# Kernel tuning notes

Hardware: AMD Instinct MI355X
Metric: run time of the kernel (lower is better)

## Reference

```python
import jax, jax.numpy as jnp
import numpy as np

NUM_HEADS = 16
NEG = -1e9


def setup_inputs() -> dict:
    key = jax.random.key(0)
    k_x, k_w1, k_w2, k_b, k_p = jax.random.split(key, 5)
    B, T, C = 4, 2048, 1024
    x = jax.random.normal(k_x, (B, T, C), dtype=jnp.float32)
    # nn.Linear default init ~ U(-1/sqrt(fan_in), 1/sqrt(fan_in)); stored as (in, out) for x @ W
    s = 1.0 / np.sqrt(C)
    Wqkv = jax.random.uniform(k_w1, (C, 3 * C), minval=-s, maxval=s, dtype=jnp.float32)
    Wout = jax.random.uniform(k_w2, (C, C), minval=-s, maxval=s, dtype=jnp.float32)
    bout = jax.random.uniform(k_b, (C,), minval=-s, maxval=s, dtype=jnp.float32)
    perm = jax.random.permutation(k_p, T).astype(jnp.int32)
    return {"x": x, "Wqkv": Wqkv, "Wout": Wout, "bout": bout, "perm": perm}


def reference(x, Wqkv, Wout, bout, perm):
    B, T, C = x.shape
    H = NUM_HEADS
    D = C // H
    qkv = x @ Wqkv                                   # [B,T,3C]
    q, k, v = jnp.split(qkv, 3, axis=-1)
    q = q.reshape(B, T, H, D)
    k = k.reshape(B, T, H, D)
    v = v.reshape(B, T, H, D)
    scale = 1.0 / jnp.sqrt(jnp.asarray(D, dtype=x.dtype))
    scores = jnp.einsum('bqhd,bkhd->bhqk', q, k) * scale   # [B,H,T,T]
    # permuted causal mask: allowed[i, j] = tril[i, perm[j]] = (perm[j] <= i)
    i = jnp.arange(T)[:, None]
    bias = jnp.where(perm[None, :] <= i, 0.0, NEG).astype(x.dtype)  # [T,T]
    attn = jax.nn.softmax(scores + bias[None, None, :, :], axis=-1)
    out = jnp.einsum('bhqk,bkhd->bqhd', attn, v).reshape(B, T, C)
    return out @ Wout + bout
```

## Files before the change

### kernel.cpp

```cpp
#include <hip/hip_runtime.h>
#include <stdint.h>
#include <stddef.h>

#define BSZ   4
#define TSEQ  2048
#define CDIM  1024
#define HEADS 16
#define DHEAD 64

typedef __attribute__((ext_vector_type(8))) short v8s;
typedef __attribute__((ext_vector_type(4))) float v4f;

__device__ __forceinline__ v4f mfma16(v8s a, v8s b, v4f c) {
  return __builtin_amdgcn_mfma_f32_16x16x32_bf16(a, b, c, 0, 0, 0);
}

__device__ __forceinline__ short f2bf(float f) {
  union { float f; uint32_t u; } v; v.f = f;
  uint32_t r = (v.u + 0x7FFFu + ((v.u >> 16) & 1u)) >> 16;
  return (short)(uint16_t)r;
}

__device__ __forceinline__ uint32_t cvt_pk_bf16(float lo, float hi) {
  uint32_t r;
  asm("v_cvt_pk_bf16_f32 %0, %1, %2" : "=v"(r) : "v"(lo), "v"(hi));
  return r;
}

__device__ __forceinline__ void gl_lds16(const void* g, void* l) {
  __builtin_amdgcn_global_load_lds((const __attribute__((address_space(1))) void*)g,
                                   (__attribute__((address_space(3))) void*)l, 16, 0, 0);
}

#define BARw __builtin_amdgcn_s_barrier()
#define LGKM0 do { asm volatile("s_waitcnt lgkmcnt(0)" ::: "memory"); \
                   __builtin_amdgcn_sched_barrier(0); } while (0)

__global__ __launch_bounds__(256) void k_convert(const float* __restrict__ in,
                                                 short* __restrict__ out, int n) {
  int i = (blockIdx.x * 256 + threadIdx.x) * 4;
  if (i >= n) return;
  float4 v = *(const float4*)(in + i);
  short4 o;
  o.x = f2bf(v.x); o.y = f2bf(v.y); o.z = f2bf(v.z); o.w = f2bf(v.w);
  *(short4*)(out + i) = o;
}

__global__ __launch_bounds__(256) void k_transpose_conv(const float* __restrict__ in,
                                                        short* __restrict__ out,
                                                        int R, int C) {
  __shared__ float tile[32][33];
  int c0 = blockIdx.x * 32, r0 = blockIdx.y * 32;
  int tx = threadIdx.x, ty = threadIdx.y;
  #pragma unroll
  for (int i = ty; i < 32; i += 8)
    tile[i][tx] = in[(size_t)(r0 + i) * C + c0 + tx];
  __syncthreads();
  #pragma unroll
  for (int i = ty; i < 32; i += 8)
    out[(size_t)(c0 + i) * R + r0 + tx] = f2bf(tile[tx][i]);
}

__global__ __launch_bounds__(256) void k_vt(const short* __restrict__ Vs,
                                            short* __restrict__ Vt) {
  __shared__ short tl[64][72];
  const int t0 = blockIdx.x * 64, h = blockIdx.y, b = blockIdx.z;
  const int row = threadIdx.x >> 2, c4 = threadIdx.x & 3;
  const short* src = Vs + (size_t)(b * TSEQ + t0 + row) * CDIM + h * DHEAD;
  #pragma unroll
  for (int it = 0; it < 2; ++it) {
    int ch = c4 + it * 4;
    *(v8s*)&tl[row][ch * 8] = *(const v8s*)(src + ch * 8);
  }
  __syncthreads();
  short* dst = Vt + ((size_t)(b * HEADS + h) * DHEAD + row) * TSEQ + t0;
  #pragma unroll
  for (int it = 0; it < 2; ++it) {
    int ch = c4 + it * 4;
    v8s o;
    #pragma unroll
    for (int j = 0; j < 8; ++j) o[j] = tl[ch * 8 + j][row];
    *(v8s*)(dst + ch * 8) = o;
  }
}

__global__ __launch_bounds__(512, 2) void k_gemm_qkv(const short* __restrict__ A,
                                                     const short* __restrict__ Wt,
                                                     const int* __restrict__ perm,
                                                     short* __restrict__ QK,
                                                     short* __restrict__ Vs) {
  __shared__ __align__(16) short Alds[2][256 * 64];
  __shared__ __align__(16) short Blds[2][256 * 64];
  const int l = threadIdx.x & 63, w = threadIdx.x >> 6;
  const int lr = l & 15, lg = l >> 4;
  const int wm = w >> 2, wn = w & 3;
  const int bid = blockIdx.x;
  const int swz = (bid & 7) * 48 + (bid >> 3);
  const int by = swz / 12, bx = swz - by * 12;
  const int row0 = by * 256, col0 = bx * 256;

  v4f acc[8][4];
  #pragma unroll
  for (int i = 0; i < 8; ++i)
    #pragma unroll
    for (int j = 0; j < 4; ++j) acc[i][j] = (v4f){0.f, 0.f, 0.f, 0.f};

  const int rowoff = w * 8 + (l >> 3);
  const int gch = ((l & 7) ^ (l >> 3)) * 16;
  const char* Asrc = (const char*)A  + (size_t)(row0 + rowoff) * 2048 + gch;
  const char* Bsrc = (const char*)Wt + (size_t)(col0 + rowoff) * 2048 + gch;
  char* AL = (char*)&Alds[0][0];
  char* BL = (char*)&Blds[0][0];
  const int sdst = w * 1024;

  auto SA = [&](int kt, int h, int d) {
    char* dst = AL + d * 32768 + h * 16384 + sdst;
    const char* s = Asrc + (size_t)(h * 128) * 2048 + kt * 128;
    gl_lds16(s, dst);
    gl_lds16(s + (size_t)64 * 2048, dst + 8192);
  };
  auto SB = [&](int kt, int h, int d) {
    char* dst = BL + d * 32768 + h * 16384 + sdst;
    const char* s = Bsrc + (size_t)(h * 128) * 2048 + kt * 128;
    gl_lds16(s, dst);
    gl_lds16(s + (size_t)64 * 2048, dst + 8192);
  };

  const int rsw = (lr & 7) * 16;
  const int koff0 = (lg * 16) ^ rsw;
  const int koff1 = ((4 + lg) * 16) ^ rsw;
  const int abase = (wm * 128 + lr) * 128;
  const int bbase = (wn * 64 + lr) * 128;

  v8s af[4][2], bf[4][2];
  auto RDA = [&](int d, int ih) {
    const char* base = AL + d * 32768 + abase + ih * 8192;
    #pragma unroll
    for (int ii = 0; ii < 4; ++ii) {
      af[ii][0] = *(const v8s*)(base + ii * 2048 + koff0);
      af[ii][1] = *(const v8s*)(base + ii * 2048 + koff1);
    }
  };
  auto RDB = [&](int d) {
    const char* base = BL + d * 32768 + bbase;
    #pragma unroll
    for (int j = 0; j < 4; ++j) {
      bf[j][0] = *(const v8s*)(base + j * 2048 + koff0);
      bf[j][1] = *(const v8s*)(base + j * 2048 + koff1);
    }
  };

#define MMC(IH, JH)                                                            \
  do {                                                                         \
    __builtin_amdgcn_s_setprio(1);                                             \
    _Pragma("unroll")                                                          \
    for (int kk = 0; kk < 2; ++kk)                                             \
      _Pragma("unroll")                                                        \
      for (int ii = 0; ii < 4; ++ii)                                           \
        _Pragma("unroll")                                                      \
        for (int jj = 0; jj < 2; ++jj)                                         \
          acc[(IH) * 4 + ii][(JH) * 2 + jj] =                                  \
              mfma16(af[ii][kk], bf[(JH) * 2 + jj][kk],                        \
                     acc[(IH) * 4 + ii][(JH) * 2 + jj]);                       \
    __builtin_amdgcn_s_setprio(0);                                             \
  } while (0)

  SB(0, 0, 0); SB(0, 1, 0); SA(0, 0, 0); SA(0, 1, 0);
  SB(1, 0, 1); SB(1, 1, 1); SA(1, 0, 1); SA(1, 1, 1);
  asm volatile("s_waitcnt vmcnt(8)" ::: "memory");
  BARw;

  for (int i = 0; i < 8; ++i) {
    const int kt2 = 2 * i + 2, kt3 = 2 * i + 3;
    const bool st = (i < 7);
    RDA(0, 0); RDB(0);
    BARw; LGKM0; MMC(0, 0); BARw;
    if (st) SB(kt2, 0, 0);
    BARw; MMC(0, 1); BARw;
    RDA(0, 1); if (st) SB(kt2, 1, 0);
    BARw; LGKM0; MMC(1, 0); BARw;
    if (st) { SA(kt2, 0, 0); asm volatile("s_waitcnt vmcnt(6)" ::: "memory"); }
    else    { asm volatile("s_waitcnt vmcnt(0)" ::: "memory"); }
    BARw; MMC(1, 1); BARw;
    RDA(1, 0); RDB(1); if (st) SA(kt2, 1, 0);
    BARw; LGKM0; MMC(0, 0); BARw;
    if (st) SB(kt3, 0, 1);
    BARw; MMC(0, 1); BARw;
    RDA(1, 1); if (st) SB(kt3, 1, 1);
    BARw; LGKM0; MMC(1, 0); BARw;
    if (st) {
      SA(kt3, 0, 1); SA(kt3, 1, 1);
      asm volatile("s_waitcnt vmcnt(8)" ::: "memory");
    }
    BARw; MMC(1, 1); BARw;
  }
#undef MMC

  const int region = (col0 + wn * 64) >> 10;
  if (region == 0) {
    #pragma unroll
    for (int i = 0; i < 8; ++i) {
      int rowb = row0 + wm * 128 + i * 16 + lg * 4;
      #pragma unroll
      for (int j = 0; j < 4; ++j) {
        int col = col0 + wn * 64 + j * 16 + lr;
        #pragma unroll
        for (int r = 0; r < 4; ++r)
          QK[(size_t)(rowb + r) * 2048 + col] = f2bf(acc[i][j][r]);
      }
    }
  } else if (region == 1) {
    #pragma unroll
    for (int i = 0; i < 8; ++i) {
      int rowb = row0 + wm * 128 + i * 16 + lg * 4;
      int prow[4];
      #pragma unroll
      for (int r = 0; r < 4; ++r) {
        int t = (rowb + r) & 2047;
        prow[r] = ((rowb + r) - t) + perm[t];
      }
      #pragma unroll
      for (int j = 0; j < 4; ++j) {
        int col = col0 + wn * 64 + j * 16 + lr;
        #pragma unroll
        for (int r = 0; r < 4; ++r)
          QK[(size_t)prow[r] * 2048 + col] = f2bf(acc[i][j][r]);
      }
    }
  } else {
    #pragma unroll
    for (int i = 0; i < 8; ++i) {
      int rowb = row0 + wm * 128 + i * 16 + lg * 4;
      int prow[4];
      #pragma unroll
      for (int r = 0; r < 4; ++r) {
        int t = (rowb + r) & 2047;
        prow[r] = ((rowb + r) - t) + perm[t];
      }
      #pragma unroll
      for (int j = 0; j < 4; ++j) {
        int vc = col0 + wn * 64 + j * 16 + lr - 2048;
        #pragma unroll
        for (int r = 0; r < 4; ++r)
          Vs[(size_t)prow[r] * CDIM + vc] = f2bf(acc[i][j][r]);
      }
    }
  }
}

__global__ __launch_bounds__(256) void k_gemm_out(const short* __restrict__ A,
                                                  const short* __restrict__ Wt,
                                                  const float* __restrict__ bias,
                                                  float* __restrict__ out) {
  __shared__ __align__(16) short As[3][128 * 32];
  __shared__ __align__(16) short Bs[3][128 * 32];
  int l = threadIdx.x & 63, w = threadIdx.x >> 6;
  int lr = l & 15, lg = l >> 4;
  int row0 = blockIdx.y * 128, col0 = blockIdx.x * 128;
  int wr = (w >> 1) * 64, wc = (w & 1) * 64;
  v4f acc[4][4];
  #pragma unroll
  for (int i = 0; i < 4; ++i)
    #pragma unroll
    for (int j = 0; j < 4; ++j) acc[i][j] = (v4f){0.f, 0.f, 0.f, 0.f};

  const short* Ag = A  + (size_t)(row0 + w * 32 + (l >> 2)) * CDIM + (l & 3) * 8;
  const short* Bg = Wt + (size_t)(col0 + w * 32 + (l >> 2)) * CDIM + (l & 3) * 8;
  const int so = (w * 32) * 32;

  auto STAGE = [&](int it, int bf) {
    int k0 = it * 32;
    gl_lds16(Ag + k0, &As[bf][so]);
    gl_lds16(Ag + k0 + 16 * CDIM, &As[bf][so + 16 * 32]);
    gl_lds16(Bg + k0, &Bs[bf][so]);
    gl_lds16(Bg + k0 + 16 * CDIM, &Bs[bf][so + 16 * 32]);
  };

  auto BODY = [&](int it, int cur) {
    if (it < 31) asm volatile("s_waitcnt vmcnt(4)" ::: "memory");
    else         asm volatile("s_waitcnt vmcnt(0)" ::: "memory");
    __builtin_amdgcn_s_barrier();
    if (it < 30) STAGE(it + 2, (cur + 2) % 3);
    v8s af[4], bfr[4];
    #pragma unroll
    for (int i = 0; i < 4; ++i) af[i] = *(const v8s*)&As[cur][(wr + i * 16 + lr) * 32 + lg * 8];
    #pragma unroll
    for (int j = 0; j < 4; ++j) bfr[j] = *(const v8s*)&Bs[cur][(wc + j * 16 + lr) * 32 + lg * 8];
    __builtin_amdgcn_s_setprio(1);
    #pragma unroll
    for (int i = 0; i < 4; ++i)
      #pragma unroll
      for (int j = 0; j < 4; ++j) acc[i][j] = mfma16(af[i], bfr[j], acc[i][j]);
    __builtin_amdgcn_s_setprio(0);
  };

  STAGE(0, 0);
  STAGE(1, 1);
  for (int it = 0; it < 30; it += 3) {
    BODY(it, 0); BODY(it + 1, 1); BODY(it + 2, 2);
  }
  BODY(30, 0);
  BODY(31, 1);

  #pragma unroll
  for (int i = 0; i < 4; ++i) {
    int rowb = row0 + wr + i * 16 + lg * 4;
    #pragma unroll
    for (int j = 0; j < 4; ++j) {
      int col = col0 + wc + j * 16 + lr;
      float bv = bias[col];
      #pragma unroll
      for (int r = 0; r < 4; ++r)
        out[(size_t)(rowb + r) * CDIM + col] = acc[i][j][r] + bv;
    }
  }
}

__global__ __launch_bounds__(512) void k_flash(const short* __restrict__ QK,
                                               const short* __restrict__ Vt,
                                               short* __restrict__ O) {
  __shared__ __align__(16) short Kbuf[3][64 * 64];
  __shared__ __align__(16) short Vbuf[3][64 * 64];
  __shared__ __align__(16) short plds[8][32 * 64];
  const int l = threadIdx.x & 63, w = threadIdx.x >> 6;
  const int lr = l & 15, lg = l >> 4;
  const int n = blockIdx.x;
  const int u = n & 255;
  const int h = u & 15;
  const int b = (u >> 4) & 3;
  const int qi = u >> 6;
  const int qb = (n < 256) ? (7 - qi) : qi;
  const int q0 = qb * 256 + w * 32;
  const int nt = 4 * qb + 4;
  const float C1 = 0.18033688011112042f;

  const short* Qb = QK + (size_t)(b * TSEQ + q0) * 2048 + h * DHEAD;
  v8s aq[2][2];
  #pragma unroll
  for (int hh = 0; hh < 2; ++hh) {
    aq[hh][0] = *(const v8s*)(Qb + (size_t)(hh * 16 + lr) * 2048 + lg * 8);
    aq[hh][1] = *(const v8s*)(Qb + (size_t)(hh * 16 + lr) * 2048 + 32 + lg * 8);
  }

  v8s ones;
  #pragma unroll
  for (int i = 0; i < 8; ++i) ones[i] = (short)0x3F80;

  v4f Oacc[2][4], sacc[2];
  #pragma unroll
  for (int hh = 0; hh < 2; ++hh) {
    sacc[hh] = (v4f){0.f, 0.f, 0.f, 0.f};
    #pragma unroll
    for (int d = 0; d < 4; ++d) Oacc[hh][d] = (v4f){0.f, 0.f, 0.f, 0.f};
  }

  const char* Ksrc = (const char*)QK + (size_t)(b * TSEQ) * 4096 + 2048 + (size_t)h * 128;
  const char* Vsrc = (const char*)Vt + (size_t)((b * HEADS + h) * DHEAD) * 4096;
  const int srow = w * 8 + (l >> 3);
  const int csw  = ((l & 7) ^ (l >> 3)) * 16;

  auto STAGE = [&](int kt, int bf) {
    char* kd = (char*)&Kbuf[bf][0] + w * 1024;
    char* vd = (char*)&Vbuf[bf][0] + w * 1024;
    gl_lds16(Ksrc + ((size_t)kt * 64 + srow) * 4096 + csw, kd);
    gl_lds16(Vsrc + (size_t)srow * 4096 + (size_t)kt * 128 + csw, vd);
  };

  STAGE(0, 0);
  if (nt > 1) STAGE(1, 1);
  const int x16 = (lr & 7) * 16;
  char* pb = (char*)&plds[w][0];
  const int e7 = lr & 7;

  for (int kt = 0; kt < nt; ++kt) {
    const int cur = kt % 3;
    if (kt + 1 < nt) asm volatile("s_waitcnt vmcnt(2)" ::: "memory");
    else             asm volatile("s_waitcnt vmcnt(0)" ::: "memory");
    __builtin_amdgcn_s_barrier();
    if (kt + 2 < nt) STAGE(kt + 2, (kt + 2) % 3);

    if (kt * 64 <= q0 + 31) {
      const char* Kc = (const char*)&Kbuf[cur][0];
      const char* Vc = (const char*)&Vbuf[cur][0];

      v4f S[2][4];
      __builtin_amdgcn_s_setprio(1);
      #pragma unroll
      for (int g = 0; g < 4; ++g) {
        const char* rp = Kc + (g * 16 + lr) * 128;
        v8s k0 = *(const v8s*)(rp + ((lg * 16) ^ x16));
        v8s k1 = *(const v8s*)(rp + ((64 + lg * 16) ^ x16));
        #pragma unroll
        for (int hh = 0; hh < 2; ++hh) {
          v4f z = (v4f){0.f, 0.f, 0.f, 0.f};
          z = mfma16(k0, aq[hh][0], z);
          S[hh][g] = mfma16(k1, aq[hh][1], z);
        }
      }
      __builtin_amdgcn_s_setprio(0);

      if (kt * 64 + 63 <= q0) {
        #pragma unroll
        for (int hh = 0; hh < 2; ++hh) {
          char* rowp = pb + (hh * 16 + lr) * 128 + 8 * (lg & 1);
          #pragma unroll
          for (int g = 0; g < 4; ++g) {
            float p0 = __builtin_exp2f(fmaf(S[hh][g][0], C1, -8.0f));
            float p1 = __builtin_exp2f(fmaf(S[hh][g][1], C1, -8.0f));
            float p2 = __builtin_exp2f(fmaf(S[hh][g][2], C1, -8.0f));
            float p3 = __builtin_exp2f(fmaf(S[hh][g][3], C1, -8.0f));
            uint2 wv;
            wv.x = cvt_pk_bf16(p0, p1);
            wv.y = cvt_pk_bf16(p2, p3);
            *(uint2*)(rowp + (((2 * g + (lg >> 1)) ^ e7) << 4)) = wv;
          }
        }
      } else {
        const int kg0 = kt * 64 + lg * 4;
        #pragma unroll
        for (int hh = 0; hh < 2; ++hh) {
          const int irow = q0 + hh * 16 + lr;
          char* rowp = pb + (hh * 16 + lr) * 128 + 8 * (lg & 1);
          #pragma unroll
          for (int g = 0; g < 4; ++g) {
            float p[4];
            #pragma unroll
            for (int r = 0; r < 4; ++r) {
              float e = __builtin_exp2f(fmaf(S[hh][g][r], C1, -8.0f));
              p[r] = (kg0 + g * 16 + r <= irow) ? e : 0.0f;
            }
            uint2 wv;
            wv.x = cvt_pk_bf16(p[0], p[1]);
            wv.y = cvt_pk_bf16(p[2], p[3]);
            *(uint2*)(rowp + (((2 * g + (lg >> 1)) ^ e7) << 4)) = wv;
          }
        }
      }
      asm volatile("s_waitcnt lgkmcnt(0)" ::: "memory");
      __builtin_amdgcn_sched_barrier(0);

      v8s ap[2][2];
      #pragma unroll
      for (int hh = 0; hh < 2; ++hh) {
        const char* rowp = pb + (hh * 16 + lr) * 128;
        ap[hh][0] = *(const v8s*)(rowp + ((lg ^ e7) << 4));
        ap[hh][1] = *(const v8s*)(rowp + (((4 + lg) ^ e7) << 4));
      }
      __builtin_amdgcn_s_setprio(1);
      #pragma unroll
      for (int hh = 0; hh < 2; ++hh) {
        sacc[hh] = mfma16(ap[hh][0], ones, sacc[hh]);
        sacc[hh] = mfma16(ap[hh][1], ones, sacc[hh]);
      }
      #pragma unroll
      for (int dk = 0; dk < 4; ++dk) {
        const char* vp = Vc + (dk * 16 + lr) * 128;
        v8s bv0 = *(const v8s*)(vp + ((lg * 16) ^ x16));
        v8s bv1 = *(const v8s*)(vp + ((64 + lg * 16) ^ x16));
        #pragma unroll
        for (int hh = 0; hh < 2; ++hh) {
          Oacc[hh][dk] = mfma16(ap[hh][0], bv0, Oacc[hh][dk]);
          Oacc[hh][dk] = mfma16(ap[hh][1], bv1, Oacc[hh][dk]);
        }
      }
      __builtin_amdgcn_s_setprio(0);
    }
  }

  #pragma unroll
  for (int hh = 0; hh < 2; ++hh) {
    float inv[4];
    #pragma unroll
    for (int r = 0; r < 4; ++r) inv[r] = 1.0f / sacc[hh][r];
    #pragma unroll
    for (int dk = 0; dk < 4; ++dk)
      #pragma unroll
      for (int r = 0; r < 4; ++r) {
        int row = q0 + hh * 16 + lg * 4 + r;
        int col = h * DHEAD + dk * 16 + lr;
        O[(size_t)(b * TSEQ + row) * CDIM + col] = f2bf(Oacc[hh][dk][r] * inv[r]);
      }
  }
}

extern "C" void kernel_launch(void* const* d_in, const int* in_sizes, int n_in,
                              void* d_out, int out_size, void* d_ws, size_t ws_size,
                              hipStream_t stream) {
  const float* x    = (const float*)d_in[0];
  const float* Wqkv = (const float*)d_in[1];
  const float* Wout = (const float*)d_in[2];
  const float* bout = (const float*)d_in[3];
  const int*   perm = (const int*)d_in[4];
  float* out = (float*)d_out;

  uint8_t* ws = (uint8_t*)d_ws;
  const size_t NTOK = (size_t)BSZ * TSEQ;
  size_t off = 0;
  short* Xb    = (short*)(ws + off); off += NTOK * CDIM * 2;
  short* Wqkvt = (short*)(ws + off); off += (size_t)3 * CDIM * CDIM * 2;
  short* Woutt = (short*)(ws + off); off += (size_t)CDIM * CDIM * 2;
  short* QKb   = (short*)(ws + off); off += NTOK * 2048 * 2;
  short* Vtb   = (short*)(ws + off); off += NTOK * CDIM * 2;
  short* Obuf  = (short*)(ws + off); off += NTOK * CDIM * 2;
  short* Vsb   = Obuf;

  {
    int n = (int)(NTOK * CDIM);
    k_convert<<<n / (256 * 4), 256, 0, stream>>>(x, Xb, n);
  }
  k_transpose_conv<<<dim3(3 * CDIM / 32, CDIM / 32), dim3(32, 8), 0, stream>>>(Wqkv, Wqkvt, CDIM, 3 * CDIM);
  k_transpose_conv<<<dim3(CDIM / 32, CDIM / 32), dim3(32, 8), 0, stream>>>(Wout, Woutt, CDIM, CDIM);
  k_gemm_qkv<<<dim3((NTOK / 256) * (3 * CDIM / 256)), 512, 0, stream>>>(Xb, Wqkvt, perm, QKb, Vsb);
  k_vt<<<dim3(TSEQ / 64, HEADS, BSZ), 256, 0, stream>>>(Vsb, Vtb);
  k_flash<<<dim3(512), 512, 0, stream>>>(QKb, Vtb, Obuf);
  k_gemm_out<<<dim3(CDIM / 128, NTOK / 128), 256, 0, stream>>>(Obuf, Woutt, bout, out);
}
```

Baseline: 201.4 us.

## Load K/V fragments directly from global memory in flash kernel, smaller blocks

The flash attention kernel stops staging K and V tiles through a triple-buffered shared-memory pipeline with barriers. Each wave now reads its MFMA K and V fragments straight from global memory (relying on L2/cache reuse) and loops only over its own causal extent. Blocks shrink to 256 threads covering 128 query rows, launched as 1024 blocks with a new load-balancing order. This removes barriers and shared-memory traffic but exposes global-load latency in the MFMA loop, and K/V data is no longer shared across the waves of a block.

New measurement: 244.6 us. +21.4%, slower.

```diff
diff --git a/kernel.cpp b/kernel.cpp
--- a/kernel.cpp
+++ b/kernel.cpp
@@ -316,22 +316,21 @@
   }
 }
 
-__global__ __launch_bounds__(512) void k_flash(const short* __restrict__ QK,
+__global__ __launch_bounds__(256) void k_flash(const short* __restrict__ QK,
                                                const short* __restrict__ Vt,
                                                short* __restrict__ O) {
-  __shared__ __align__(16) short Kbuf[3][64 * 64];
-  __shared__ __align__(16) short Vbuf[3][64 * 64];
-  __shared__ __align__(16) short plds[8][32 * 64];
+  __shared__ __align__(16) short plds[4][32 * 64];
   const int l = threadIdx.x & 63, w = threadIdx.x >> 6;
   const int lr = l & 15, lg = l >> 4;
   const int n = blockIdx.x;
+  const int g = n >> 8;
   const int u = n & 255;
   const int h = u & 15;
   const int b = (u >> 4) & 3;
-  const int qi = u >> 6;
-  const int qb = (n < 256) ? (7 - qi) : qi;
-  const int q0 = qb * 256 + w * 32;
-  const int nt = 4 * qb + 4;
+  const int s = u >> 6;
+  const int qb = (g == 0) ? (15 - s) : (g == 1) ? s : (g == 2) ? (11 - s) : (4 + s);
+  const int q0 = qb * 128 + w * 32;
+  const int nt_w = ((q0 + 31) >> 6) + 1;
   const float C1 = 0.18033688011112042f;
 
   const short* Qb = QK + (size_t)(b * TSEQ + q0) * 2048 + h * DHEAD;
@@ -354,116 +353,92 @@
     for (int d = 0; d < 4; ++d) Oacc[hh][d] = (v4f){0.f, 0.f, 0.f, 0.f};
   }
 
-  const char* Ksrc = (const char*)QK + (size_t)(b * TSEQ) * 4096 + 2048 + (size_t)h * 128;
-  const char* Vsrc = (const char*)Vt + (size_t)((b * HEADS + h) * DHEAD) * 4096;
-  const int srow = w * 8 + (l >> 3);
-  const int csw  = ((l & 7) ^ (l >> 3)) * 16;
-
-  auto STAGE = [&](int kt, int bf) {
-    char* kd = (char*)&Kbuf[bf][0] + w * 1024;
-    char* vd = (char*)&Vbuf[bf][0] + w * 1024;
-    gl_lds16(Ksrc + ((size_t)kt * 64 + srow) * 4096 + csw, kd);
-    gl_lds16(Vsrc + (size_t)srow * 4096 + (size_t)kt * 128 + csw, vd);
-  };
-
-  STAGE(0, 0);
-  if (nt > 1) STAGE(1, 1);
-  const int x16 = (lr & 7) * 16;
+  const short* Klane = QK + (size_t)(b * TSEQ) * 2048 + 1024 + h * DHEAD
+                          + (size_t)lr * 2048 + lg * 8;
+  const short* Vlane = Vt + (size_t)((b * HEADS + h) * DHEAD) * TSEQ
+                          + (size_t)lr * TSEQ + lg * 8;
+
   char* pb = (char*)&plds[w][0];
   const int e7 = lr & 7;
 
-  for (int kt = 0; kt < nt; ++kt) {
-    const int cur = kt % 3;
-    if (kt + 1 < nt) asm volatile("s_waitcnt vmcnt(2)" ::: "memory");
-    else             asm volatile("s_waitcnt vmcnt(0)" ::: "memory");
-    __builtin_amdgcn_s_barrier();
-    if (kt + 2 < nt) STAGE(kt + 2, (kt + 2) % 3);
-
-    if (kt * 64 <= q0 + 31) {
-      const char* Kc = (const char*)&Kbuf[cur][0];
-      const char* Vc = (const char*)&Vbuf[cur][0];
-
-      v4f S[2][4];
-      __builtin_amdgcn_s_setprio(1);
-      #pragma unroll
-      for (int g = 0; g < 4; ++g) {
-        const char* rp = Kc + (g * 16 + lr) * 128;
-        v8s k0 = *(const v8s*)(rp + ((lg * 16) ^ x16));
-        v8s k1 = *(const v8s*)(rp + ((64 + lg * 16) ^ x16));
+  for (int kt = 0; kt < nt_w; ++kt) {
+    const short* Kt = Klane + (size_t)kt * 64 * 2048;
+    const short* Vtp = Vlane + kt * 64;
+
+    v4f S[2][4];
+    #pragma unroll
+    for (int g4 = 0; g4 < 4; ++g4) {
+      v8s k0 = *(const v8s*)(Kt + (size_t)g4 * 16 * 2048);
+      v8s k1 = *(const v8s*)(Kt + (size_t)g4 * 16 * 2048 + 32);
+      #pragma unroll
+      for (int hh = 0; hh < 2; ++hh) {
+        v4f z = (v4f){0.f, 0.f, 0.f, 0.f};
+        z = mfma16(k0, aq[hh][0], z);
+        S[hh][g4] = mfma16(k1, aq[hh][1], z);
+      }
+    }
+
+    if (kt * 64 + 63 <= q0) {
+      #pragma unroll
+      for (int hh = 0; hh < 2; ++hh) {
+        char* rowp = pb + (hh * 16 + lr) * 128 + 8 * (lg & 1);
         #pragma unroll
-        for (int hh = 0; hh < 2; ++hh) {
-          v4f z = (v4f){0.f, 0.f, 0.f, 0.f};
-          z = mfma16(k0, aq[hh][0], z);
-          S[hh][g] = mfma16(k1, aq[hh][1], z);
+        for (int g4 = 0; g4 < 4; ++g4) {
+          float p0 = __builtin_exp2f(fmaf(S[hh][g4][0], C1, -8.0f));
+          float p1 = __builtin_exp2f(fmaf(S[hh][g4][1], C1, -8.0f));
+          float p2 = __builtin_exp2f(fmaf(S[hh][g4][2], C1, -8.0f));
+          float p3 = __builtin_exp2f(fmaf(S[hh][g4][3], C1, -8.0f));
+          uint2 wv;
+          wv.x = cvt_pk_bf16(p0, p1);
+          wv.y = cvt_pk_bf16(p2, p3);
+          *(uint2*)(rowp + (((2 * g4 + (lg >> 1)) ^ e7) << 4)) = wv;
         }
       }
-      __builtin_amdgcn_s_setprio(0);
-
-      if (kt * 64 + 63 <= q0) {
+    } else {
+      const int kg0 = kt * 64 + lg * 4;
+      #pragma unroll
+      for (int hh = 0; hh < 2; ++hh) {
+        const int irow = q0 + hh * 16 + lr;
+        char* rowp = pb + (hh * 16 + lr) * 128 + 8 * (lg & 1);
         #pragma unroll
-        for (int hh = 0; hh < 2; ++hh) {
-          char* rowp = pb + (hh * 16 + lr) * 128 + 8 * (lg & 1);
+        for (int g4 = 0; g4 < 4; ++g4) {
+          float p[4];
           #pragma unroll
-          for (int g = 0; g < 4; ++g) {
-            float p0 = __builtin_exp2f(fmaf(S[hh][g][0], C1, -8.0f));
-            float p1 = __builtin_exp2f(fmaf(S[hh][g][1], C1, -8.0f));
-            float p2 = __builtin_exp2f(fmaf(S[hh][g][2], C1, -8.0f));
-            float p3 = __builtin_exp2f(fmaf(S[hh][g][3], C1, -8.0f));
-            uint2 wv;
-            wv.x = cvt_pk_bf16(p0, p1);
-            wv.y = cvt_pk_bf16(p2, p3);
-            *(uint2*)(rowp + (((2 * g + (lg >> 1)) ^ e7) << 4)) = wv;
+          for (int r = 0; r < 4; ++r) {
+            float e = __builtin_exp2f(fmaf(S[hh][g4][r], C1, -8.0f));
+            p[r] = (kg0 + g4 * 16 + r <= irow) ? e : 0.0f;
           }
+          uint2 wv;
+          wv.x = cvt_pk_bf16(p[0], p[1]);
+          wv.y = cvt_pk_bf16(p[2], p[3]);
+          *(uint2*)(rowp + (((2 * g4 + (lg >> 1)) ^ e7) << 4)) = wv;
         }
-      } else {
-        const int kg0 = kt * 64 + lg * 4;
-        #pragma unroll
-        for (int hh = 0; hh < 2; ++hh) {
-          const int irow = q0 + hh * 16 + lr;
-          char* rowp = pb + (hh * 16 + lr) * 128 + 8 * (lg & 1);
-          #pragma unroll
-          for (int g = 0; g < 4; ++g) {
-            float p[4];
-            #pragma unroll
-            for (int r = 0; r < 4; ++r) {
-              float e = __builtin_exp2f(fmaf(S[hh][g][r], C1, -8.0f));
-              p[r] = (kg0 + g * 16 + r <= irow) ? e : 0.0f;
-            }
-            uint2 wv;
-            wv.x = cvt_pk_bf16(p[0], p[1]);
-            wv.y = cvt_pk_bf16(p[2], p[3]);
-            *(uint2*)(rowp + (((2 * g + (lg >> 1)) ^ e7) << 4)) = wv;
-          }
-        }
-      }
-      asm volatile("s_waitcnt lgkmcnt(0)" ::: "memory");
-      __builtin_amdgcn_sched_barrier(0);
-
-      v8s ap[2][2];
+      }
+    }
+    asm volatile("s_waitcnt lgkmcnt(0)" ::: "memory");
+    __builtin_amdgcn_sched_barrier(0);
+
+    v8s ap[2][2];
+    #pragma unroll
+    for (int hh = 0; hh < 2; ++hh) {
+      const char* rowp = pb + (hh * 16 + lr) * 128;
+      ap[hh][0] = *(const v8s*)(rowp + ((lg ^ e7) << 4));
+      ap[hh][1] = *(const v8s*)(rowp + (((4 + lg) ^ e7) << 4));
+    }
+    #pragma unroll
+    for (int hh = 0; hh < 2; ++hh) {
+      sacc[hh] = mfma16(ap[hh][0], ones, sacc[hh]);
+      sacc[hh] = mfma16(ap[hh][1], ones, sacc[hh]);
+    }
+    #pragma unroll
+    for (int dk = 0; dk < 4; ++dk) {
+      v8s bv0 = *(const v8s*)(Vtp + (size_t)dk * 16 * TSEQ);
+      v8s bv1 = *(const v8s*)(Vtp + (size_t)dk * 16 * TSEQ + 32);
       #pragma unroll
       for (int hh = 0; hh < 2; ++hh) {
-        const char* rowp = pb + (hh * 16 + lr) * 128;
-        ap[hh][0] = *(const v8s*)(rowp + ((lg ^ e7) << 4));
-        ap[hh][1] = *(const v8s*)(rowp + (((4 + lg) ^ e7) << 4));
-      }
-      __builtin_amdgcn_s_setprio(1);
-      #pragma unroll
-      for (int hh = 0; hh < 2; ++hh) {
-        sacc[hh] = mfma16(ap[hh][0], ones, sacc[hh]);
-        sacc[hh] = mfma16(ap[hh][1], ones, sacc[hh]);
-      }
-      #pragma unroll
-      for (int dk = 0; dk < 4; ++dk) {
-        const char* vp = Vc + (dk * 16 + lr) * 128;
-        v8s bv0 = *(const v8s*)(vp + ((lg * 16) ^ x16));
-        v8s bv1 = *(const v8s*)(vp + ((64 + lg * 16) ^ x16));
-        #pragma unroll
-        for (int hh = 0; hh < 2; ++hh) {
-          Oacc[hh][dk] = mfma16(ap[hh][0], bv0, Oacc[hh][dk]);
-          Oacc[hh][dk] = mfma16(ap[hh][1], bv1, Oacc[hh][dk]);
-        }
-      }
-      __builtin_amdgcn_s_setprio(0);
+        Oacc[hh][dk] = mfma16(ap[hh][0], bv0, Oacc[hh][dk]);
+        Oacc[hh][dk] = mfma16(ap[hh][1], bv1, Oacc[hh][dk]);
+      }
     }
   }
 
@@ -512,6 +487,6 @@
   k_transpose_conv<<<dim3(CDIM / 32, CDIM / 32), dim3(32, 8), 0, stream>>>(Wout, Woutt, CDIM, CDIM);
   k_gemm_qkv<<<dim3((NTOK / 256) * (3 * CDIM / 256)), 512, 0, stream>>>(Xb, Wqkvt, perm, QKb, Vsb);
   k_vt<<<dim3(TSEQ / 64, HEADS, BSZ), 256, 0, stream>>>(Vsb, Vtb);
-  k_flash<<<dim3(512), 512, 0, stream>>>(QKb, Vtb, Obuf);
+  k_flash<<<dim3(1024), 256, 0, stream>>>(QKb, Vtb, Obuf);
   k_gemm_out<<<dim3(CDIM / 128, NTOK / 128), 256, 0, stream>>>(Obuf, Woutt, bout, out);
 }
```

## Give each flash-attention wave 64 query rows with 4 waves per block

Applied to the files above, without the earlier changes.

The flash kernel now runs 4 waves of 256 threads instead of 8 waves of 512. Each wave owns 64 query rows, handled as two 32-row passes over every K/V tile, and each thread stages two 16-byte chunks per matrix per tile. Each K/V fragment read from LDS now serves more query rows, and fewer waves contend at the per-tile barrier. The cost is more accumulator registers per thread and fewer waves to hide latency, which may reduce occupancy.

After: 247.3 us. +22.8%, slower.

```diff
diff --git a/kernel.cpp b/kernel.cpp
--- a/kernel.cpp
+++ b/kernel.cpp
@@ -316,12 +316,12 @@
   }
 }
 
-__global__ __launch_bounds__(512) void k_flash(const short* __restrict__ QK,
+__global__ __launch_bounds__(256) void k_flash(const short* __restrict__ QK,
                                                const short* __restrict__ Vt,
                                                short* __restrict__ O) {
   __shared__ __align__(16) short Kbuf[3][64 * 64];
   __shared__ __align__(16) short Vbuf[3][64 * 64];
-  __shared__ __align__(16) short plds[8][32 * 64];
+  __shared__ __align__(16) short plds[4][64 * 64];
   const int l = threadIdx.x & 63, w = threadIdx.x >> 6;
   const int lr = l & 15, lg = l >> 4;
   const int n = blockIdx.x;
@@ -330,28 +330,28 @@
   const int b = (u >> 4) & 3;
   const int qi = u >> 6;
   const int qb = (n < 256) ? (7 - qi) : qi;
-  const int q0 = qb * 256 + w * 32;
+  const int q0 = qb * 256 + w * 64;
   const int nt = 4 * qb + 4;
   const float C1 = 0.18033688011112042f;
 
   const short* Qb = QK + (size_t)(b * TSEQ + q0) * 2048 + h * DHEAD;
-  v8s aq[2][2];
-  #pragma unroll
-  for (int hh = 0; hh < 2; ++hh) {
-    aq[hh][0] = *(const v8s*)(Qb + (size_t)(hh * 16 + lr) * 2048 + lg * 8);
-    aq[hh][1] = *(const v8s*)(Qb + (size_t)(hh * 16 + lr) * 2048 + 32 + lg * 8);
+  v8s aq[4][2];
+  #pragma unroll
+  for (int ph = 0; ph < 4; ++ph) {
+    aq[ph][0] = *(const v8s*)(Qb + (size_t)(ph * 16 + lr) * 2048 + lg * 8);
+    aq[ph][1] = *(const v8s*)(Qb + (size_t)(ph * 16 + lr) * 2048 + 32 + lg * 8);
   }
 
   v8s ones;
   #pragma unroll
   for (int i = 0; i < 8; ++i) ones[i] = (short)0x3F80;
 
-  v4f Oacc[2][4], sacc[2];
-  #pragma unroll
-  for (int hh = 0; hh < 2; ++hh) {
-    sacc[hh] = (v4f){0.f, 0.f, 0.f, 0.f};
-    #pragma unroll
-    for (int d = 0; d < 4; ++d) Oacc[hh][d] = (v4f){0.f, 0.f, 0.f, 0.f};
+  v4f Oacc[4][4], sacc[4];
+  #pragma unroll
+  for (int ph = 0; ph < 4; ++ph) {
+    sacc[ph] = (v4f){0.f, 0.f, 0.f, 0.f};
+    #pragma unroll
+    for (int d = 0; d < 4; ++d) Oacc[ph][d] = (v4f){0.f, 0.f, 0.f, 0.f};
   }
 
   const char* Ksrc = (const char*)QK + (size_t)(b * TSEQ) * 4096 + 2048 + (size_t)h * 128;
@@ -362,123 +362,133 @@
   auto STAGE = [&](int kt, int bf) {
     char* kd = (char*)&Kbuf[bf][0] + w * 1024;
     char* vd = (char*)&Vbuf[bf][0] + w * 1024;
-    gl_lds16(Ksrc + ((size_t)kt * 64 + srow) * 4096 + csw, kd);
-    gl_lds16(Vsrc + (size_t)srow * 4096 + (size_t)kt * 128 + csw, vd);
+    const char* ks = Ksrc + ((size_t)kt * 64 + srow) * 4096 + csw;
+    const char* vs = Vsrc + (size_t)srow * 4096 + (size_t)kt * 128 + csw;
+    gl_lds16(ks, kd);
+    gl_lds16(ks + (size_t)32 * 4096, kd + 4096);
+    gl_lds16(vs, vd);
+    gl_lds16(vs + (size_t)32 * 4096, vd + 4096);
   };
 
   STAGE(0, 0);
-  if (nt > 1) STAGE(1, 1);
+  STAGE(1, 1);
   const int x16 = (lr & 7) * 16;
   char* pb = (char*)&plds[w][0];
   const int e7 = lr & 7;
 
   for (int kt = 0; kt < nt; ++kt) {
     const int cur = kt % 3;
-    if (kt + 1 < nt) asm volatile("s_waitcnt vmcnt(2)" ::: "memory");
+    if (kt + 1 < nt) asm volatile("s_waitcnt vmcnt(4)" ::: "memory");
     else             asm volatile("s_waitcnt vmcnt(0)" ::: "memory");
     __builtin_amdgcn_s_barrier();
     if (kt + 2 < nt) STAGE(kt + 2, (kt + 2) % 3);
 
-    if (kt * 64 <= q0 + 31) {
+    if (kt * 64 <= q0 + 63) {
       const char* Kc = (const char*)&Kbuf[cur][0];
       const char* Vc = (const char*)&Vbuf[cur][0];
 
-      v4f S[2][4];
-      __builtin_amdgcn_s_setprio(1);
-      #pragma unroll
-      for (int g = 0; g < 4; ++g) {
-        const char* rp = Kc + (g * 16 + lr) * 128;
-        v8s k0 = *(const v8s*)(rp + ((lg * 16) ^ x16));
-        v8s k1 = *(const v8s*)(rp + ((64 + lg * 16) ^ x16));
-        #pragma unroll
-        for (int hh = 0; hh < 2; ++hh) {
-          v4f z = (v4f){0.f, 0.f, 0.f, 0.f};
-          z = mfma16(k0, aq[hh][0], z);
-          S[hh][g] = mfma16(k1, aq[hh][1], z);
-        }
-      }
-      __builtin_amdgcn_s_setprio(0);
-
-      if (kt * 64 + 63 <= q0) {
-        #pragma unroll
-        for (int hh = 0; hh < 2; ++hh) {
-          char* rowp = pb + (hh * 16 + lr) * 128 + 8 * (lg & 1);
+      #pragma unroll
+      for (int p = 0; p < 2; ++p) {
+        const int q0p = q0 + p * 32;
+        if (kt * 64 > q0p + 31) continue;
+
+        v4f S[2][4];
+        __builtin_amdgcn_s_setprio(1);
+        #pragma unroll
+        for (int g4 = 0; g4 < 4; ++g4) {
+          const char* rp = Kc + (g4 * 16 + lr) * 128;
+          v8s k0 = *(const v8s*)(rp + ((lg * 16) ^ x16));
+          v8s k1 = *(const v8s*)(rp + ((64 + lg * 16) ^ x16));
           #pragma unroll
-          for (int g = 0; g < 4; ++g) {
-            float p0 = __builtin_exp2f(fmaf(S[hh][g][0], C1, -8.0f));
-            float p1 = __builtin_exp2f(fmaf(S[hh][g][1], C1, -8.0f));
-            float p2 = __builtin_exp2f(fmaf(S[hh][g][2], C1, -8.0f));
-            float p3 = __builtin_exp2f(fmaf(S[hh][g][3], C1, -8.0f));
-            uint2 wv;
-            wv.x = cvt_pk_bf16(p0, p1);
-            wv.y = cvt_pk_bf16(p2, p3);
-            *(uint2*)(rowp + (((2 * g + (lg >> 1)) ^ e7) << 4)) = wv;
+          for (int hh = 0; hh < 2; ++hh) {
+            v4f z = (v4f){0.f, 0.f, 0.f, 0.f};
+            z = mfma16(k0, aq[2 * p + hh][0], z);
+            S[hh][g4] = mfma16(k1, aq[2 * p + hh][1], z);
           }
         }
-      } else {
-        const int kg0 = kt * 64 + lg * 4;
-        #pragma unroll
-        for (int hh = 0; hh < 2; ++hh) {
-          const int irow = q0 + hh * 16 + lr;
-          char* rowp = pb + (hh * 16 + lr) * 128 + 8 * (lg & 1);
+        __builtin_amdgcn_s_setprio(0);
+
+        if (kt * 64 + 63 <= q0p) {
           #pragma unroll
-          for (int g = 0; g < 4; ++g) {
-            float p[4];
+          for (int hh = 0; hh < 2; ++hh) {
+            char* rowp = pb + (p * 32 + hh * 16 + lr) * 128 + 8 * (lg & 1);
             #pragma unroll
-            for (int r = 0; r < 4; ++r) {
-              float e = __builtin_exp2f(fmaf(S[hh][g][r], C1, -8.0f));
-              p[r] = (kg0 + g * 16 + r <= irow) ? e : 0.0f;
+            for (int g4 = 0; g4 < 4; ++g4) {
+              float p0 = __builtin_exp2f(fmaf(S[hh][g4][0], C1, -8.0f));
+              float p1 = __builtin_exp2f(fmaf(S[hh][g4][1], C1, -8.0f));
+              float p2 = __builtin_exp2f(fmaf(S[hh][g4][2], C1, -8.0f));
+              float p3 = __builtin_exp2f(fmaf(S[hh][g4][3], C1, -8.0f));
+              uint2 wv;
+              wv.x = cvt_pk_bf16(p0, p1);
+              wv.y = cvt_pk_bf16(p2, p3);
+              *(uint2*)(rowp + (((2 * g4 + (lg >> 1)) ^ e7) << 4)) = wv;
             }
-            uint2 wv;
-            wv.x = cvt_pk_bf16(p[0], p[1]);
-            wv.y = cvt_pk_bf16(p[2], p[3]);
-            *(uint2*)(rowp + (((2 * g + (lg >> 1)) ^ e7) << 4)) = wv;
+          }
+        } else {
+          const int kg0 = kt * 64 + lg * 4;
+          #pragma unroll
+          for (int hh = 0; hh < 2; ++hh) {
+            const int irow = q0p + hh * 16 + lr;
+            char* rowp = pb + (p * 32 + hh * 16 + lr) * 128 + 8 * (lg & 1);
+            #pragma unroll
+            for (int g4 = 0; g4 < 4; ++g4) {
+              float pv[4];
+              #pragma unroll
+              for (int r = 0; r < 4; ++r) {
+                float e = __builtin_exp2f(fmaf(S[hh][g4][r], C1, -8.0f));
+                pv[r] = (kg0 + g4 * 16 + r <= irow) ? e : 0.0f;
+              }
+              uint2 wv;
+              wv.x = cvt_pk_bf16(pv[0], pv[1]);
+              wv.y = cvt_pk_bf16(pv[2], pv[3]);
+              *(uint2*)(rowp + (((2 * g4 + (lg >> 1)) ^ e7) << 4)) = wv;
+            }
           }
         }
-      }
-      asm volatile("s_waitcnt lgkmcnt(0)" ::: "memory");
-      __builtin_amdgcn_sched_barrier(0);
-
-      v8s ap[2][2];
-      #pragma unroll
-      for (int hh = 0; hh < 2; ++hh) {
-        const char* rowp = pb + (hh * 16 + lr) * 128;
-        ap[hh][0] = *(const v8s*)(rowp + ((lg ^ e7) << 4));
-        ap[hh][1] = *(const v8s*)(rowp + (((4 + lg) ^ e7) << 4));
-      }
-      __builtin_amdgcn_s_setprio(1);
-      #pragma unroll
-      for (int hh = 0; hh < 2; ++hh) {
-        sacc[hh] = mfma16(ap[hh][0], ones, sacc[hh]);
-        sacc[hh] = mfma16(ap[hh][1], ones, sacc[hh]);
-      }
-      #pragma unroll
-      for (int dk = 0; dk < 4; ++dk) {
-        const char* vp = Vc + (dk * 16 + lr) * 128;
-        v8s bv0 = *(const v8s*)(vp + ((lg * 16) ^ x16));
-        v8s bv1 = *(const v8s*)(vp + ((64 + lg * 16) ^ x16));
+        asm volatile("s_waitcnt lgkmcnt(0)" ::: "memory");
+        __builtin_amdgcn_sched_barrier(0);
+
+        v8s ap[2][2];
         #pragma unroll
         for (int hh = 0; hh < 2; ++hh) {
-          Oacc[hh][dk] = mfma16(ap[hh][0], bv0, Oacc[hh][dk]);
-          Oacc[hh][dk] = mfma16(ap[hh][1], bv1, Oacc[hh][dk]);
+          const char* rowp = pb + (p * 32 + hh * 16 + lr) * 128;
+          ap[hh][0] = *(const v8s*)(rowp + ((lg ^ e7) << 4));
+          ap[hh][1] = *(const v8s*)(rowp + (((4 + lg) ^ e7) << 4));
         }
-      }
-      __builtin_amdgcn_s_setprio(0);
-    }
-  }
-
-  #pragma unroll
-  for (int hh = 0; hh < 2; ++hh) {
+        __builtin_amdgcn_s_setprio(1);
+        #pragma unroll
+        for (int hh = 0; hh < 2; ++hh) {
+          sacc[2 * p + hh] = mfma16(ap[hh][0], ones, sacc[2 * p + hh]);
+          sacc[2 * p + hh] = mfma16(ap[hh][1], ones, sacc[2 * p + hh]);
+        }
+        #pragma unroll
+        for (int dk = 0; dk < 4; ++dk) {
+          const char* vp = Vc + (dk * 16 + lr) * 128;
+          v8s bv0 = *(const v8s*)(vp + ((lg * 16) ^ x16));
+          v8s bv1 = *(const v8s*)(vp + ((64 + lg * 16) ^ x16));
+          #pragma unroll
+          for (int hh = 0; hh < 2; ++hh) {
+            Oacc[2 * p + hh][dk] = mfma16(ap[hh][0], bv0, Oacc[2 * p + hh][dk]);
+            Oacc[2 * p + hh][dk] = mfma16(ap[hh][1], bv1, Oacc[2 * p + hh][dk]);
+          }
+        }
+        __builtin_amdgcn_s_setprio(0);
+      }
+    }
+  }
+
+  #pragma unroll
+  for (int ph = 0; ph < 4; ++ph) {
     float inv[4];
     #pragma unroll
-    for (int r = 0; r < 4; ++r) inv[r] = 1.0f / sacc[hh][r];
+    for (int r = 0; r < 4; ++r) inv[r] = 1.0f / sacc[ph][r];
     #pragma unroll
     for (int dk = 0; dk < 4; ++dk)
       #pragma unroll
       for (int r = 0; r < 4; ++r) {
-        int row = q0 + hh * 16 + lg * 4 + r;
+        int row = q0 + ph * 16 + lg * 4 + r;
         int col = h * DHEAD + dk * 16 + lr;
-        O[(size_t)(b * TSEQ + row) * CDIM + col] = f2bf(Oacc[hh][dk][r] * inv[r]);
+        O[(size_t)(b * TSEQ + row) * CDIM + col] = f2bf(Oacc[ph][dk][r] * inv[r]);
       }
   }
 }
@@ -512,6 +522,6 @@
   k_transpose_conv<<<dim3(CDIM / 32, CDIM / 32), dim3(32, 8), 0, stream>>>(Wout, Woutt, CDIM, CDIM);
   k_gemm_qkv<<<dim3((NTOK / 256) * (3 * CDIM / 256)), 512, 0, stream>>>(Xb, Wqkvt, perm, QKb, Vsb);
   k_vt<<<dim3(TSEQ / 64, HEADS, BSZ), 256, 0, stream>>>(Vsb, Vtb);
-  k_flash<<<dim3(512), 512, 0, stream>>>(QKb, Vtb, Obuf);
+  k_flash<<<dim3(512), 256, 0, stream>>>(QKb, Vtb, Obuf);
   k_gemm_out<<<dim3(CDIM / 128, NTOK / 128), 256, 0, stream>>>(Obuf, Woutt, bout, out);
 }
```

## Software-pipeline flash loop: overlap next tile's QK^T with current softmax/PV

Applied to the files above, without the earlier changes.

Restructures the attention main loop into a two-stage software pipeline. The QK^T MFMAs for the next K tile now run alongside the softmax and PV of the current tile, using ping-pong score registers. It also adds an occupancy hint to launch_bounds. The intent is to hide exp/LDS latency behind matrix work. The cost is extra registers for a second score tile and vmcnt(0) waits that drain the prefetch, which may reduce memory overlap.

After: 438.3 us. 118% more time.

```diff
diff --git a/kernel.cpp b/kernel.cpp
--- a/kernel.cpp
+++ b/kernel.cpp
@@ -316,9 +316,9 @@
   }
 }
 
-__global__ __launch_bounds__(512) void k_flash(const short* __restrict__ QK,
-                                               const short* __restrict__ Vt,
-                                               short* __restrict__ O) {
+__global__ __launch_bounds__(512, 4) void k_flash(const short* __restrict__ QK,
+                                                  const short* __restrict__ Vt,
+                                                  short* __restrict__ O) {
   __shared__ __align__(16) short Kbuf[3][64 * 64];
   __shared__ __align__(16) short Vbuf[3][64 * 64];
   __shared__ __align__(16) short plds[8][32 * 64];
@@ -366,105 +366,115 @@
     gl_lds16(Vsrc + (size_t)srow * 4096 + (size_t)kt * 128 + csw, vd);
   };
 
-  STAGE(0, 0);
-  if (nt > 1) STAGE(1, 1);
   const int x16 = (lr & 7) * 16;
   char* pb = (char*)&plds[w][0];
   const int e7 = lr & 7;
 
-  for (int kt = 0; kt < nt; ++kt) {
-    const int cur = kt % 3;
-    if (kt + 1 < nt) asm volatile("s_waitcnt vmcnt(2)" ::: "memory");
-    else             asm volatile("s_waitcnt vmcnt(0)" ::: "memory");
-    __builtin_amdgcn_s_barrier();
-    if (kt + 2 < nt) STAGE(kt + 2, (kt + 2) % 3);
-
-    if (kt * 64 <= q0 + 31) {
-      const char* Kc = (const char*)&Kbuf[cur][0];
-      const char* Vc = (const char*)&Vbuf[cur][0];
-
-      v4f S[2][4];
-      __builtin_amdgcn_s_setprio(1);
-      #pragma unroll
-      for (int g = 0; g < 4; ++g) {
-        const char* rp = Kc + (g * 16 + lr) * 128;
-        v8s k0 = *(const v8s*)(rp + ((lg * 16) ^ x16));
-        v8s k1 = *(const v8s*)(rp + ((64 + lg * 16) ^ x16));
+  auto QKT = [&](int t, v4f (&S)[2][4]) {
+    const char* Kc = (const char*)&Kbuf[t % 3][0];
+    __builtin_amdgcn_s_setprio(1);
+    #pragma unroll
+    for (int g = 0; g < 4; ++g) {
+      const char* rp = Kc + (g * 16 + lr) * 128;
+      v8s k0 = *(const v8s*)(rp + ((lg * 16) ^ x16));
+      v8s k1 = *(const v8s*)(rp + ((64 + lg * 16) ^ x16));
+      #pragma unroll
+      for (int hh = 0; hh < 2; ++hh) {
+        v4f z = (v4f){0.f, 0.f, 0.f, 0.f};
+        z = mfma16(k0, aq[hh][0], z);
+        S[hh][g] = mfma16(k1, aq[hh][1], z);
+      }
+    }
+    __builtin_amdgcn_s_setprio(0);
+  };
+
+  auto SMPV = [&](int t, v4f (&S)[2][4]) {
+    if (t * 64 + 63 <= q0) {
+      #pragma unroll
+      for (int hh = 0; hh < 2; ++hh) {
+        char* rowp = pb + (hh * 16 + lr) * 128 + 8 * (lg & 1);
         #pragma unroll
-        for (int hh = 0; hh < 2; ++hh) {
-          v4f z = (v4f){0.f, 0.f, 0.f, 0.f};
-          z = mfma16(k0, aq[hh][0], z);
-          S[hh][g] = mfma16(k1, aq[hh][1], z);
+        for (int g = 0; g < 4; ++g) {
+          float p0 = __builtin_exp2f(fmaf(S[hh][g][0], C1, -8.0f));
+          float p1 = __builtin_exp2f(fmaf(S[hh][g][1], C1, -8.0f));
+          float p2 = __builtin_exp2f(fmaf(S[hh][g][2], C1, -8.0f));
+          float p3 = __builtin_exp2f(fmaf(S[hh][g][3], C1, -8.0f));
+          uint2 wv;
+          wv.x = cvt_pk_bf16(p0, p1);
+          wv.y = cvt_pk_bf16(p2, p3);
+          *(uint2*)(rowp + (((2 * g + (lg >> 1)) ^ e7) << 4)) = wv;
         }
       }
-      __builtin_amdgcn_s_setprio(0);
-
-      if (kt * 64 + 63 <= q0) {
+    } else {
+      const int kg0 = t * 64 + lg * 4;
+      #pragma unroll
+      for (int hh = 0; hh < 2; ++hh) {
+        const int irow = q0 + hh * 16 + lr;
+        char* rowp = pb + (hh * 16 + lr) * 128 + 8 * (lg & 1);
         #pragma unroll
-        for (int hh = 0; hh < 2; ++hh) {
-          char* rowp = pb + (hh * 16 + lr) * 128 + 8 * (lg & 1);
+        for (int g = 0; g < 4; ++g) {
+          float p[4];
           #pragma unroll
-          for (int g = 0; g < 4; ++g) {
-            float p0 = __builtin_exp2f(fmaf(S[hh][g][0], C1, -8.0f));
-            float p1 = __builtin_exp2f(fmaf(S[hh][g][1], C1, -8.0f));
-            float p2 = __builtin_exp2f(fmaf(S[hh][g][2], C1, -8.0f));
-            float p3 = __builtin_exp2f(fmaf(S[hh][g][3], C1, -8.0f));
-            uint2 wv;
-            wv.x = cvt_pk_bf16(p0, p1);
-            wv.y = cvt_pk_bf16(p2, p3);
-            *(uint2*)(rowp + (((2 * g + (lg >> 1)) ^ e7) << 4)) = wv;
+          for (int r = 0; r < 4; ++r) {
+            float e = __builtin_exp2f(fmaf(S[hh][g][r], C1, -8.0f));
+            p[r] = (kg0 + g * 16 + r <= irow) ? e : 0.0f;
           }
+          uint2 wv;
+          wv.x = cvt_pk_bf16(p[0], p[1]);
+          wv.y = cvt_pk_bf16(p[2], p[3]);
+          *(uint2*)(rowp + (((2 * g + (lg >> 1)) ^ e7) << 4)) = wv;
         }
-      } else {
-        const int kg0 = kt * 64 + lg * 4;
-        #pragma unroll
-        for (int hh = 0; hh < 2; ++hh) {
-          const int irow = q0 + hh * 16 + lr;
-          char* rowp = pb + (hh * 16 + lr) * 128 + 8 * (lg & 1);
-          #pragma unroll
-          for (int g = 0; g < 4; ++g) {
-            float p[4];
-            #pragma unroll
-            for (int r = 0; r < 4; ++r) {
-              float e = __builtin_exp2f(fmaf(S[hh][g][r], C1, -8.0f));
-              p[r] = (kg0 + g * 16 + r <= irow) ? e : 0.0f;
-            }
-            uint2 wv;
-            wv.x = cvt_pk_bf16(p[0], p[1]);
-            wv.y = cvt_pk_bf16(p[2], p[3]);
-            *(uint2*)(rowp + (((2 * g + (lg >> 1)) ^ e7) << 4)) = wv;
-          }
-        }
-      }
-      asm volatile("s_waitcnt lgkmcnt(0)" ::: "memory");
-      __builtin_amdgcn_sched_barrier(0);
-
-      v8s ap[2][2];
+      }
+    }
+    asm volatile("s_waitcnt lgkmcnt(0)" ::: "memory");
+    __builtin_amdgcn_sched_barrier(0);
+
+    v8s ap[2][2];
+    #pragma unroll
+    for (int hh = 0; hh < 2; ++hh) {
+      const char* rowp = pb + (hh * 16 + lr) * 128;
+      ap[hh][0] = *(const v8s*)(rowp + ((lg ^ e7) << 4));
+      ap[hh][1] = *(const v8s*)(rowp + (((4 + lg) ^ e7) << 4));
+    }
+    const char* Vc = (const char*)&Vbuf[t % 3][0];
+    __builtin_amdgcn_s_setprio(1);
+    #pragma unroll
+    for (int hh = 0; hh < 2; ++hh) {
+      sacc[hh] = mfma16(ap[hh][0], ones, sacc[hh]);
+      sacc[hh] = mfma16(ap[hh][1], ones, sacc[hh]);
+    }
+    #pragma unroll
+    for (int dk = 0; dk < 4; ++dk) {
+      const char* vp = Vc + (dk * 16 + lr) * 128;
+      v8s bv0 = *(const v8s*)(vp + ((lg * 16) ^ x16));
+      v8s bv1 = *(const v8s*)(vp + ((64 + lg * 16) ^ x16));
       #pragma unroll
       for (int hh = 0; hh < 2; ++hh) {
-        const char* rowp = pb + (hh * 16 + lr) * 128;
-        ap[hh][0] = *(const v8s*)(rowp + ((lg ^ e7) << 4));
-        ap[hh][1] = *(const v8s*)(rowp + (((4 + lg) ^ e7) << 4));
-      }
-      __builtin_amdgcn_s_setprio(1);
-      #pragma unroll
-      for (int hh = 0; hh < 2; ++hh) {
-        sacc[hh] = mfma16(ap[hh][0], ones, sacc[hh]);
-        sacc[hh] = mfma16(ap[hh][1], ones, sacc[hh]);
-      }
-      #pragma unroll
-      for (int dk = 0; dk < 4; ++dk) {
-        const char* vp = Vc + (dk * 16 + lr) * 128;
-        v8s bv0 = *(const v8s*)(vp + ((lg * 16) ^ x16));
-        v8s bv1 = *(const v8s*)(vp + ((64 + lg * 16) ^ x16));
-        #pragma unroll
-        for (int hh = 0; hh < 2; ++hh) {
-          Oacc[hh][dk] = mfma16(ap[hh][0], bv0, Oacc[hh][dk]);
-          Oacc[hh][dk] = mfma16(ap[hh][1], bv1, Oacc[hh][dk]);
-        }
-      }
-      __builtin_amdgcn_s_setprio(0);
-    }
+        Oacc[hh][dk] = mfma16(ap[hh][0], bv0, Oacc[hh][dk]);
+        Oacc[hh][dk] = mfma16(ap[hh][1], bv1, Oacc[hh][dk]);
+      }
+    }
+    __builtin_amdgcn_s_setprio(0);
+  };
+
+  STAGE(0, 0);
+  STAGE(1, 1);
+  asm volatile("s_waitcnt vmcnt(2)" ::: "memory");
+  BARw;
+  v4f Sa[2][4], Sb[2][4];
+  QKT(0, Sa);
+
+  for (int i = 0; i < nt; i += 2) {
+    asm volatile("s_waitcnt vmcnt(0)" ::: "memory");
+    BARw;
+    if (i + 2 < nt) STAGE(i + 2, (i + 2) % 3);
+    if ((i + 1) * 64 <= q0 + 31) QKT(i + 1, Sb);
+    if (i * 64 <= q0 + 31) SMPV(i, Sa);
+    asm volatile("s_waitcnt vmcnt(0)" ::: "memory");
+    BARw;
+    if (i + 3 < nt) STAGE(i + 3, (i + 3) % 3);
+    if (i + 2 < nt && (i + 2) * 64 <= q0 + 31) QKT(i + 2, Sa);
+    if ((i + 1) * 64 <= q0 + 31) SMPV(i + 1, Sb);
   }
 
   #pragma unroll
```
